# Kernel optimization log

Measured on AMD Instinct MI355X. Metric: run time of the kernel, lower is better.

Reference implementation:

```python
import jax, jax.numpy as jnp
import numpy as np
import math

D = 1024
L = 4096
B = 4

def setup_inputs() -> dict:
    key = jax.random.key(0)
    ks = jax.random.split(key, 6)
    x = jax.random.normal(ks[0], (B, L, D), dtype=jnp.float32)
    base_phases = jax.random.normal(ks[1], (L, D), dtype=jnp.float32) * math.pi
    s = 1.0 / math.sqrt(D)
    W_v = jax.random.normal(ks[2], (D, D), dtype=jnp.float32) * s
    b_v = jnp.zeros((D,), dtype=jnp.float32)
    ln_g = jnp.ones((D,), dtype=jnp.float32)
    ln_b = jnp.zeros((D,), dtype=jnp.float32)
    W_o = jax.random.normal(ks[3], (D, D), dtype=jnp.float32) * s
    b_o = jnp.zeros((D,), dtype=jnp.float32)
    return {"x": x, "base_phases": base_phases, "W_v": W_v, "b_v": b_v,
            "ln_g": ln_g, "ln_b": ln_b, "W_o": W_o, "b_o": b_o}

def _layernorm(x, g, b, eps=1e-5):
    mu = jnp.mean(x, axis=-1, keepdims=True)
    var = jnp.mean(jnp.square(x - mu), axis=-1, keepdims=True)
    return (x - mu) * jax.lax.rsqrt(var + eps) * g + b

def reference(x, base_phases, W_v, b_v, ln_g, ln_b, W_o, b_o):
    Bv, Lv, Dv = x.shape
    phases = base_phases[:Lv][None, :, :]          # [1, L, D]
    cosp, sinp = jnp.cos(phases), jnp.sin(phases)
    value = jnp.einsum('bld,ed->ble', x, W_v) + b_v  # Linear(D,D)
    mem_real = jnp.cumsum(value * cosp, axis=1)
    mem_imag = jnp.cumsum(value * sinp, axis=1)
    retrieved = (mem_real * cosp + mem_imag * sinp) / math.sqrt(Dv)
    out = jnp.einsum('bld,ed->ble', _layernorm(retrieved, ln_g, ln_b), W_o) + b_o
    return x + out
```

## Files before the change

### kernel.cpp

```cpp
#include <hip/hip_runtime.h>
#include <stdint.h>


#define D_DIM 1024
#define L_DIM 4096
#define B_DIM 4
#define M_DIM (B_DIM * L_DIM)
#define CHUNK 64
#define NCH (L_DIM / CHUNK)
#define NT 16

typedef __attribute__((ext_vector_type(8))) short short8;
typedef __attribute__((ext_vector_type(4))) float f32x4;

__device__ __forceinline__ float bf2f(uint32_t h) {
  union { uint32_t u; float f; } x; x.u = h << 16; return x.f;
}
__device__ __forceinline__ uint16_t f2bf(float f) {
  union { float f; uint32_t u; } x; x.f = f;
  uint32_t u = x.u;
  u += 0x7fffu + ((u >> 16) & 1u);
  return (uint16_t)(u >> 16);
}

__global__ void k_f2bf(const float* __restrict__ in, uint16_t* __restrict__ out, int n) {
  int i = (blockIdx.x * 256 + threadIdx.x) * 8;
  if (i >= n) return;
  float4 a = *(const float4*)(in + i);
  float4 b = *(const float4*)(in + i + 4);
  ushort4 o0 = { f2bf(a.x), f2bf(a.y), f2bf(a.z), f2bf(a.w) };
  ushort4 o1 = { f2bf(b.x), f2bf(b.y), f2bf(b.z), f2bf(b.w) };
  *(ushort4*)(out + i) = o0;
  *(ushort4*)(out + i + 4) = o1;
}

__global__ void k_prep_wo(const float* __restrict__ Wo, const float* __restrict__ g,
                          const float* __restrict__ bln, const float* __restrict__ bo,
                          uint16_t* __restrict__ wob, float* __restrict__ u,
                          float* __restrict__ vb) {
  int e = blockIdx.x;
  int tid = threadIdx.x;
  int d = tid * 4;
  float4 w  = *(const float4*)(Wo + (size_t)e * D_DIM + d);
  float4 gg = *(const float4*)(g + d);
  float4 bb = *(const float4*)(bln + d);
  float gw0 = gg.x * w.x, gw1 = gg.y * w.y, gw2 = gg.z * w.z, gw3 = gg.w * w.w;
  ushort4 o = { f2bf(gw0), f2bf(gw1), f2bf(gw2), f2bf(gw3) };
  *(ushort4*)(wob + (size_t)e * D_DIM + d) = o;
  float su = gw0 + gw1 + gw2 + gw3;
  float sv = bb.x * w.x + bb.y * w.y + bb.z * w.z + bb.w * w.w;
#pragma unroll
  for (int off = 32; off > 0; off >>= 1) {
    su += __shfl_down(su, off);
    sv += __shfl_down(sv, off);
  }
  __shared__ float s1[4], s2[4];
  int wid = tid >> 6, lane = tid & 63;
  if (lane == 0) { s1[wid] = su; s2[wid] = sv; }
  __syncthreads();
  if (tid == 0) {
    u[e]  = s1[0] + s1[1] + s1[2] + s1[3];
    vb[e] = s2[0] + s2[1] + s2[2] + s2[3] + bo[e];
  }
}

template <int MODE>
__global__ __launch_bounds__(512, 2) void k_gemm(
    const uint16_t* __restrict__ A, const uint16_t* __restrict__ W,
    void* __restrict__ outp,
    const float* __restrict__ p0, const float* __restrict__ p1,
    const float* __restrict__ mu, const float* __restrict__ inv,
    const uint16_t* __restrict__ xres) {
  __shared__ char lds[8 * 16384];
  const int tid = threadIdx.x;
  const int lane = tid & 63;
  const int wid = tid >> 6;
  const int wm = wid >> 2;
  const int wn = wid & 3;

  const int idx = blockIdx.x;
  const int bm = (idx & 7) * 8 + ((idx >> 3) >> 2);
  const int bn = (idx >> 3) & 3;

  const int srow = tid >> 3;
  const int scb  = (tid & 7) * 16;
  const int scbs = scb ^ ((srow & 7) << 4);

#define GLL(SRC, DST)                                                            \
  __builtin_amdgcn_global_load_lds((const __attribute__((address_space(1))) void*)(SRC), \
                                   (__attribute__((address_space(3))) void*)(DST), 16, 0, 0)

#define STAGE_A(KS, HA)                                                          \
  do {                                                                           \
    char* _d = lds + ((((KS)&1) * 4 + (HA)) << 14) + tid * 16;                   \
    const char* _s = (const char*)A +                                            \
        (size_t)(bm * 256 + (HA) * 128 + srow) * 2048 + (KS) * 128 + scbs;       \
    GLL(_s, _d);                                                                 \
    GLL(_s + (size_t)64 * 2048, _d + 8192);                                      \
  } while (0)

#define STAGE_B(KS, HB)                                                          \
  do {                                                                           \
    char* _d = lds + ((((KS)&1) * 4 + 2 + (HB)) << 14) + tid * 16;               \
    const char* _s = (const char*)W +                                            \
        (size_t)(bn * 256 + (HB) * 128 + srow) * 2048 + (KS) * 128 + scbs;       \
    GLL(_s, _d);                                                                 \
    GLL(_s + (size_t)64 * 2048, _d + 8192);                                      \
  } while (0)

  const int axor = (lane & 7) << 4;
  const int afr  = lane & 15;
  const int acol = (lane >> 4) * 16;

#define LD_A(PAR, I, KK)                                                         \
  (*(const short8*)(lds + (((PAR) * 4 + wm) << 14) + ((I) * 16 + afr) * 128 +    \
                    (((KK) * 64 + acol) ^ axor)))
#define LD_B(PAR, J, KK)                                                         \
  (*(const short8*)(lds + (((PAR) * 4 + 2 + (wn >> 1)) << 14) +                  \
                    ((wn & 1) * 64 + (J) * 16 + afr) * 128 +                     \
                    (((KK) * 64 + acol) ^ axor)))

  f32x4 acc[8][4];
#pragma unroll
  for (int i = 0; i < 8; ++i)
#pragma unroll
    for (int j = 0; j < 4; ++j)
      acc[i][j] = (f32x4){0.f, 0.f, 0.f, 0.f};

  STAGE_A(0, 0); STAGE_A(0, 1);
  STAGE_B(0, 0); STAGE_B(0, 1);
  STAGE_A(1, 0); STAGE_A(1, 1);
  asm volatile("s_waitcnt vmcnt(4)" ::: "memory");
  __builtin_amdgcn_s_barrier();

  for (int ks = 0; ks < NT; ++ks) {
    const int par = ks & 1;
    short8 a0, a1, a2, a3, b0, b1, b2, b3;

    b0 = LD_B(par, 0, 0); b1 = LD_B(par, 1, 0); b2 = LD_B(par, 2, 0); b3 = LD_B(par, 3, 0);
    a0 = LD_A(par, 0, 0); a1 = LD_A(par, 1, 0); a2 = LD_A(par, 2, 0); a3 = LD_A(par, 3, 0);
    if (ks + 1 < NT) STAGE_B(ks + 1, 0);
    __builtin_amdgcn_s_barrier();
    asm volatile("s_waitcnt lgkmcnt(0)" ::: "memory");
    __builtin_amdgcn_sched_barrier(0);
    __builtin_amdgcn_s_setprio(1);
#pragma unroll
    for (int j = 0; j < 4; ++j) {
      const short8 bj = (j == 0) ? b0 : (j == 1) ? b1 : (j == 2) ? b2 : b3;
      acc[0][j] = __builtin_amdgcn_mfma_f32_16x16x32_bf16(a0, bj, acc[0][j], 0, 0, 0);
      acc[1][j] = __builtin_amdgcn_mfma_f32_16x16x32_bf16(a1, bj, acc[1][j], 0, 0, 0);
      acc[2][j] = __builtin_amdgcn_mfma_f32_16x16x32_bf16(a2, bj, acc[2][j], 0, 0, 0);
      acc[3][j] = __builtin_amdgcn_mfma_f32_16x16x32_bf16(a3, bj, acc[3][j], 0, 0, 0);
    }
    __builtin_amdgcn_s_setprio(0);
    __builtin_amdgcn_s_barrier();

    a0 = LD_A(par, 4, 0); a1 = LD_A(par, 5, 0); a2 = LD_A(par, 6, 0); a3 = LD_A(par, 7, 0);
    if (ks + 1 < NT) STAGE_B(ks + 1, 1);
    __builtin_amdgcn_s_barrier();
    asm volatile("s_waitcnt lgkmcnt(0)" ::: "memory");
    __builtin_amdgcn_sched_barrier(0);
    __builtin_amdgcn_s_setprio(1);
#pragma unroll
    for (int j = 0; j < 4; ++j) {
      const short8 bj = (j == 0) ? b0 : (j == 1) ? b1 : (j == 2) ? b2 : b3;
      acc[4][j] = __builtin_amdgcn_mfma_f32_16x16x32_bf16(a0, bj, acc[4][j], 0, 0, 0);
      acc[5][j] = __builtin_amdgcn_mfma_f32_16x16x32_bf16(a1, bj, acc[5][j], 0, 0, 0);
      acc[6][j] = __builtin_amdgcn_mfma_f32_16x16x32_bf16(a2, bj, acc[6][j], 0, 0, 0);
      acc[7][j] = __builtin_amdgcn_mfma_f32_16x16x32_bf16(a3, bj, acc[7][j], 0, 0, 0);
    }
    __builtin_amdgcn_s_setprio(0);
    __builtin_amdgcn_s_barrier();

    b0 = LD_B(par, 0, 1); b1 = LD_B(par, 1, 1); b2 = LD_B(par, 2, 1); b3 = LD_B(par, 3, 1);
    a0 = LD_A(par, 0, 1); a1 = LD_A(par, 1, 1); a2 = LD_A(par, 2, 1); a3 = LD_A(par, 3, 1);
    __builtin_amdgcn_s_barrier();
    asm volatile("s_waitcnt lgkmcnt(0)" ::: "memory");
    __builtin_amdgcn_sched_barrier(0);
    __builtin_amdgcn_s_setprio(1);
#pragma unroll
    for (int j = 0; j < 4; ++j) {
      const short8 bj = (j == 0) ? b0 : (j == 1) ? b1 : (j == 2) ? b2 : b3;
      acc[0][j] = __builtin_amdgcn_mfma_f32_16x16x32_bf16(a0, bj, acc[0][j], 0, 0, 0);
      acc[1][j] = __builtin_amdgcn_mfma_f32_16x16x32_bf16(a1, bj, acc[1][j], 0, 0, 0);
      acc[2][j] = __builtin_amdgcn_mfma_f32_16x16x32_bf16(a2, bj, acc[2][j], 0, 0, 0);
      acc[3][j] = __builtin_amdgcn_mfma_f32_16x16x32_bf16(a3, bj, acc[3][j], 0, 0, 0);
    }
    __builtin_amdgcn_s_setprio(0);
    __builtin_amdgcn_s_barrier();

    a0 = LD_A(par, 4, 1); a1 = LD_A(par, 5, 1); a2 = LD_A(par, 6, 1); a3 = LD_A(par, 7, 1);
    asm volatile("s_waitcnt lgkmcnt(0)" ::: "memory");
    __builtin_amdgcn_sched_barrier(0);
    __builtin_amdgcn_s_barrier();
    __builtin_amdgcn_sched_barrier(0);
    if (ks + 2 < NT) { STAGE_A(ks + 2, 0); STAGE_A(ks + 2, 1); }
    __builtin_amdgcn_s_setprio(1);
#pragma unroll
    for (int j = 0; j < 4; ++j) {
      const short8 bj = (j == 0) ? b0 : (j == 1) ? b1 : (j == 2) ? b2 : b3;
      acc[4][j] = __builtin_amdgcn_mfma_f32_16x16x32_bf16(a0, bj, acc[4][j], 0, 0, 0);
      acc[5][j] = __builtin_amdgcn_mfma_f32_16x16x32_bf16(a1, bj, acc[5][j], 0, 0, 0);
      acc[6][j] = __builtin_amdgcn_mfma_f32_16x16x32_bf16(a2, bj, acc[6][j], 0, 0, 0);
      acc[7][j] = __builtin_amdgcn_mfma_f32_16x16x32_bf16(a3, bj, acc[7][j], 0, 0, 0);
    }
    __builtin_amdgcn_s_setprio(0);
    if (ks == NT - 2) { asm volatile("s_waitcnt vmcnt(0)" ::: "memory"); }
    else              { asm volatile("s_waitcnt vmcnt(4)" ::: "memory"); }
    __builtin_amdgcn_s_barrier();
  }

  if (MODE == 0) {
    uint16_t* outv = (uint16_t*)outp;
    __syncthreads();
#pragma unroll
    for (int i = 0; i < 8; ++i)
#pragma unroll
      for (int r = 0; r < 4; ++r) {
        int row = wm * 128 + i * 16 + (lane >> 4) * 4 + r;
#pragma unroll
        for (int j = 0; j < 4; ++j) {
          int ncol = wn * 64 + j * 16 + (lane & 15);
          float v = acc[i][j][r] + p0[bn * 256 + ncol];
          *(uint16_t*)(lds + row * 512 + ((ncol * 2) ^ ((row & 7) << 4))) = f2bf(v);
        }
      }
    __syncthreads();
    {
      int row = tid >> 1, half = tid & 1;
      uint16_t* gdst = outv + (size_t)(bm * 256 + row) * D_DIM + bn * 256 + half * 128;
#pragma unroll
      for (int s = 0; s < 16; ++s) {
        short8 v = *(const short8*)(lds + row * 512 +
                                    ((half * 256 + s * 16) ^ ((row & 7) << 4)));
        *(short8*)(gdst + s * 8) = v;
      }
    }
  } else {
    float* outf = (float*)outp;
#pragma unroll
    for (int i = 0; i < 8; ++i)
#pragma unroll
      for (int r = 0; r < 4; ++r) {
        int m = bm * 256 + wm * 128 + i * 16 + (lane >> 4) * 4 + r;
        float im = inv[m], mm = mu[m];
#pragma unroll
        for (int j = 0; j < 4; ++j) {
          int n = bn * 256 + wn * 64 + j * 16 + (lane & 15);
          outf[(size_t)m * D_DIM + n] =
              im * acc[i][j][r] - im * mm * p0[n] + p1[n] +
              bf2f(xres[(size_t)m * D_DIM + n]);
        }
      }
  }
#undef GLL
#undef STAGE_A
#undef STAGE_B
#undef LD_A
#undef LD_B
}

__global__ void k_passA(const uint16_t* __restrict__ value, const float* __restrict__ phases,
                        float* __restrict__ pr, float* __restrict__ pi) {
  int d0 = blockIdx.x * 512 + threadIdx.x * 2;
  int c = blockIdx.y, b = blockIdx.z;
  const uint16_t* vp = value + ((size_t)(b * L_DIM + c * CHUNK)) * D_DIM + d0;
  const float* pp = phases + (size_t)(c * CHUNK) * D_DIM + d0;
  float sr0 = 0, si0 = 0, sr1 = 0, si1 = 0;
#pragma unroll 4
  for (int l = 0; l < CHUNK; ++l) {
    uint32_t vv = *(const uint32_t*)vp; vp += D_DIM;
    float2 ph = *(const float2*)pp; pp += D_DIM;
    float v0 = bf2f(vv & 0xffffu), v1 = bf2f(vv >> 16);
    float s0, c0, s1, c1;
    __sincosf(ph.x, &s0, &c0);
    __sincosf(ph.y, &s1, &c1);
    sr0 += v0 * c0; si0 += v0 * s0;
    sr1 += v1 * c1; si1 += v1 * s1;
  }
  size_t o = ((size_t)b * NCH + c) * D_DIM + d0;
  *(float2*)(pr + o) = make_float2(sr0, sr1);
  *(float2*)(pi + o) = make_float2(si0, si1);
}

__global__ void k_passB(float* __restrict__ pr, float* __restrict__ pi) {
  int d = blockIdx.x * 256 + threadIdx.x;
  int b = blockIdx.y;
  size_t base = (size_t)b * NCH * D_DIM + d;
  float r[NCH], im[NCH];
#pragma unroll
  for (int c = 0; c < NCH; ++c) r[c] = pr[base + (size_t)c * D_DIM];
#pragma unroll
  for (int c = 0; c < NCH; ++c) im[c] = pi[base + (size_t)c * D_DIM];
  float rr = 0, ri = 0;
#pragma unroll
  for (int c = 0; c < NCH; ++c) {
    float t = r[c]; r[c] = rr; rr += t;
    t = im[c]; im[c] = ri; ri += t;
  }
#pragma unroll
  for (int c = 0; c < NCH; ++c) pr[base + (size_t)c * D_DIM] = r[c];
#pragma unroll
  for (int c = 0; c < NCH; ++c) pi[base + (size_t)c * D_DIM] = im[c];
}

__global__ void k_passC(const uint16_t* __restrict__ value, const float* __restrict__ phases,
                        const float* __restrict__ pr, const float* __restrict__ pi,
                        uint16_t* __restrict__ ret) {
  int d0 = blockIdx.x * 512 + threadIdx.x * 2;
  int c = blockIdx.y, b = blockIdx.z;
  size_t o = ((size_t)b * NCH + c) * D_DIM + d0;
  float2 r0 = *(const float2*)(pr + o);
  float2 i0 = *(const float2*)(pi + o);
  float mr0 = r0.x, mr1 = r0.y, mi0 = i0.x, mi1 = i0.y;
  size_t rowoff = ((size_t)(b * L_DIM + c * CHUNK)) * D_DIM + d0;
  const uint16_t* vp = value + rowoff;
  uint16_t* rp = ret + rowoff;
  const float* pp = phases + (size_t)(c * CHUNK) * D_DIM + d0;
  const float isd = 0.03125f;
#pragma unroll 4
  for (int l = 0; l < CHUNK; ++l) {
    uint32_t vv = *(const uint32_t*)vp; vp += D_DIM;
    float2 ph = *(const float2*)pp; pp += D_DIM;
    float v0 = bf2f(vv & 0xffffu), v1 = bf2f(vv >> 16);
    float s0, c0, s1, c1;
    __sincosf(ph.x, &s0, &c0);
    __sincosf(ph.y, &s1, &c1);
    mr0 += v0 * c0; mi0 += v0 * s0;
    mr1 += v1 * c1; mi1 += v1 * s1;
    float o0 = (mr0 * c0 + mi0 * s0) * isd;
    float o1 = (mr1 * c1 + mi1 * s1) * isd;
    *(uint32_t*)rp = (uint32_t)f2bf(o0) | ((uint32_t)f2bf(o1) << 16);
    rp += D_DIM;
  }
}

__global__ void k_stats(const uint16_t* __restrict__ ret, float* __restrict__ mu,
                        float* __restrict__ inv) {
  int m = blockIdx.x, tid = threadIdx.x;
  ushort4 v = *(const ushort4*)(ret + (size_t)m * D_DIM + tid * 4);
  float f0 = bf2f(v.x), f1 = bf2f(v.y), f2_ = bf2f(v.z), f3 = bf2f(v.w);
  float s = f0 + f1 + f2_ + f3;
  float ss = f0 * f0 + f1 * f1 + f2_ * f2_ + f3 * f3;
#pragma unroll
  for (int off = 32; off > 0; off >>= 1) {
    s += __shfl_down(s, off);
    ss += __shfl_down(ss, off);
  }
  __shared__ float a1[4], a2[4];
  int wid = tid >> 6, lane = tid & 63;
  if (lane == 0) { a1[wid] = s; a2[wid] = ss; }
  __syncthreads();
  if (tid == 0) {
    float S = a1[0] + a1[1] + a1[2] + a1[3];
    float SS = a2[0] + a2[1] + a2[2] + a2[3];
    float mm = S * (1.0f / 1024.0f);
    float var = SS * (1.0f / 1024.0f) - mm * mm;
    mu[m] = mm;
    inv[m] = rsqrtf(var + 1e-5f);
  }
}

extern "C" void kernel_launch(void* const* d_in, const int* in_sizes, int n_in,
                              void* d_out, int out_size, void* d_ws, size_t ws_size,
                              hipStream_t stream) {
  const float* x      = (const float*)d_in[0];
  const float* phases = (const float*)d_in[1];
  const float* Wv     = (const float*)d_in[2];
  const float* bv     = (const float*)d_in[3];
  const float* lng    = (const float*)d_in[4];
  const float* lnb    = (const float*)d_in[5];
  const float* Wo     = (const float*)d_in[6];
  const float* bo     = (const float*)d_in[7];
  float* out = (float*)d_out;

  char* ws = (char*)d_ws;
  uint16_t* xb    = (uint16_t*)(ws);
  uint16_t* value = (uint16_t*)(ws + (32ull << 20));
  uint16_t* wv    = (uint16_t*)(ws + (64ull << 20));
  uint16_t* wob   = (uint16_t*)(ws + (66ull << 20));
  float* pr       = (float*)(ws + (68ull << 20));
  float* pi       = (float*)(ws + (69ull << 20));
  float* u        = (float*)(ws + (70ull << 20));
  float* vb       = (float*)(ws + (70ull << 20) + 4096);
  float* mu       = (float*)(ws + (71ull << 20));
  float* inv      = (float*)(ws + (72ull << 20));
  uint16_t* retr  = value;

  k_f2bf<<<(M_DIM * D_DIM) / 8 / 256, 256, 0, stream>>>(x, xb, M_DIM * D_DIM);
  k_f2bf<<<(D_DIM * D_DIM) / 8 / 256, 256, 0, stream>>>(Wv, wv, D_DIM * D_DIM);
  k_prep_wo<<<D_DIM, 256, 0, stream>>>(Wo, lng, lnb, bo, wob, u, vb);
  k_gemm<0><<<(M_DIM / 256) * (D_DIM / 256), 512, 0, stream>>>(
      xb, wv, value, bv, nullptr, nullptr, nullptr, nullptr);
  k_passA<<<dim3(2, NCH, B_DIM), 256, 0, stream>>>(value, phases, pr, pi);
  k_passB<<<dim3(D_DIM / 256, B_DIM), 256, 0, stream>>>(pr, pi);
  k_passC<<<dim3(2, NCH, B_DIM), 256, 0, stream>>>(value, phases, pr, pi, retr);
  k_stats<<<M_DIM, 256, 0, stream>>>(retr, mu, inv);
  k_gemm<1><<<(M_DIM / 256) * (D_DIM / 256), 512, 0, stream>>>(
      retr, wob, out, u, vb, mu, inv, xb);
}
```

Baseline: 152.6 us.

## Merge prep kernels and restructure GEMM LDS loads for deeper prefetch

The three preprocessing launches (x and Wv bf16 conversion, Wo folding) become a single kernel that dispatches work by block index, removing two launch gaps. In the GEMM main loop, both k-halves of the A and B fragments are now read from LDS up front and waited on with partial lgkmcnt counts, so the MFMAs on the first half can start while the second half's reads are still in flight. Both global B stages are issued together and fewer workgroup barriers are used per iteration. This raises register pressure from the extra fragment registers and depends on the LDS read counters being ordered as the partial waits assume.

```diff
diff --git a/kernel.cpp b/kernel.cpp
--- a/kernel.cpp
+++ b/kernel.cpp
@@ -23,23 +23,28 @@
   return (uint16_t)(u >> 16);
 }
 
-__global__ void k_f2bf(const float* __restrict__ in, uint16_t* __restrict__ out, int n) {
-  int i = (blockIdx.x * 256 + threadIdx.x) * 8;
-  if (i >= n) return;
-  float4 a = *(const float4*)(in + i);
-  float4 b = *(const float4*)(in + i + 4);
-  ushort4 o0 = { f2bf(a.x), f2bf(a.y), f2bf(a.z), f2bf(a.w) };
-  ushort4 o1 = { f2bf(b.x), f2bf(b.y), f2bf(b.z), f2bf(b.w) };
-  *(ushort4*)(out + i) = o0;
-  *(ushort4*)(out + i + 4) = o1;
-}
-
-__global__ void k_prep_wo(const float* __restrict__ Wo, const float* __restrict__ g,
-                          const float* __restrict__ bln, const float* __restrict__ bo,
-                          uint16_t* __restrict__ wob, float* __restrict__ u,
-                          float* __restrict__ vb) {
-  int e = blockIdx.x;
+__global__ void k_prep(const float* __restrict__ x, const float* __restrict__ Wv,
+                       const float* __restrict__ Wo, const float* __restrict__ g,
+                       const float* __restrict__ bln, const float* __restrict__ bo,
+                       uint16_t* __restrict__ xb, uint16_t* __restrict__ wv,
+                       uint16_t* __restrict__ wob, float* __restrict__ u,
+                       float* __restrict__ vb) {
+  int blk = blockIdx.x;
   int tid = threadIdx.x;
+  if (blk < 8192 + 512) {
+    const float* in = (blk < 8192) ? x : Wv;
+    uint16_t* outp = (blk < 8192) ? xb : wv;
+    int base = (blk < 8192) ? blk : (blk - 8192);
+    int i = (base * 256 + tid) * 8;
+    float4 a = *(const float4*)(in + i);
+    float4 b = *(const float4*)(in + i + 4);
+    ushort4 o0 = { f2bf(a.x), f2bf(a.y), f2bf(a.z), f2bf(a.w) };
+    ushort4 o1 = { f2bf(b.x), f2bf(b.y), f2bf(b.z), f2bf(b.w) };
+    *(ushort4*)(outp + i) = o0;
+    *(ushort4*)(outp + i + 4) = o1;
+    return;
+  }
+  int e = blk - 8704;
   int d = tid * 4;
   float4 w  = *(const float4*)(Wo + (size_t)e * D_DIM + d);
   float4 gg = *(const float4*)(g + d);
@@ -120,6 +125,8 @@
                     ((wn & 1) * 64 + (J) * 16 + afr) * 128 +                     \
                     (((KK) * 64 + acol) ^ axor)))
 
+#define MFMA(AV, BV, CV) __builtin_amdgcn_mfma_f32_16x16x32_bf16(AV, BV, CV, 0, 0, 0)
+
   f32x4 acc[8][4];
 #pragma unroll
   for (int i = 0; i < 8; ++i)
@@ -135,61 +142,57 @@
 
   for (int ks = 0; ks < NT; ++ks) {
     const int par = ks & 1;
-    short8 a0, a1, a2, a3, b0, b1, b2, b3;
-
-    b0 = LD_B(par, 0, 0); b1 = LD_B(par, 1, 0); b2 = LD_B(par, 2, 0); b3 = LD_B(par, 3, 0);
-    a0 = LD_A(par, 0, 0); a1 = LD_A(par, 1, 0); a2 = LD_A(par, 2, 0); a3 = LD_A(par, 3, 0);
-    if (ks + 1 < NT) STAGE_B(ks + 1, 0);
+    short8 A00, A01, A02, A03, A10, A11, A12, A13;
+    short8 B00, B01, B02, B03, B10, B11, B12, B13;
+
+    B00 = LD_B(par, 0, 0); B01 = LD_B(par, 1, 0); B02 = LD_B(par, 2, 0); B03 = LD_B(par, 3, 0);
+    A00 = LD_A(par, 0, 0); A01 = LD_A(par, 1, 0); A02 = LD_A(par, 2, 0); A03 = LD_A(par, 3, 0);
+    __builtin_amdgcn_sched_barrier(0);
+    B10 = LD_B(par, 0, 1); B11 = LD_B(par, 1, 1); B12 = LD_B(par, 2, 1); B13 = LD_B(par, 3, 1);
+    A10 = LD_A(par, 0, 1); A11 = LD_A(par, 1, 1); A12 = LD_A(par, 2, 1); A13 = LD_A(par, 3, 1);
+    __builtin_amdgcn_sched_barrier(0);
+    if (ks + 1 < NT) { STAGE_B(ks + 1, 0); STAGE_B(ks + 1, 1); }
     __builtin_amdgcn_s_barrier();
+    asm volatile("s_waitcnt lgkmcnt(8)" ::: "memory");
+    __builtin_amdgcn_sched_barrier(0);
+    __builtin_amdgcn_s_setprio(1);
+#pragma unroll
+    for (int j = 0; j < 4; ++j) {
+      const short8 bj = (j == 0) ? B00 : (j == 1) ? B01 : (j == 2) ? B02 : B03;
+      acc[0][j] = MFMA(A00, bj, acc[0][j]);
+      acc[1][j] = MFMA(A01, bj, acc[1][j]);
+      acc[2][j] = MFMA(A02, bj, acc[2][j]);
+      acc[3][j] = MFMA(A03, bj, acc[3][j]);
+    }
     asm volatile("s_waitcnt lgkmcnt(0)" ::: "memory");
     __builtin_amdgcn_sched_barrier(0);
-    __builtin_amdgcn_s_setprio(1);
 #pragma unroll
     for (int j = 0; j < 4; ++j) {
-      const short8 bj = (j == 0) ? b0 : (j == 1) ? b1 : (j == 2) ? b2 : b3;
-      acc[0][j] = __builtin_amdgcn_mfma_f32_16x16x32_bf16(a0, bj, acc[0][j], 0, 0, 0);
-      acc[1][j] = __builtin_amdgcn_mfma_f32_16x16x32_bf16(a1, bj, acc[1][j], 0, 0, 0);
-      acc[2][j] = __builtin_amdgcn_mfma_f32_16x16x32_bf16(a2, bj, acc[2][j], 0, 0, 0);
-      acc[3][j] = __builtin_amdgcn_mfma_f32_16x16x32_bf16(a3, bj, acc[3][j], 0, 0, 0);
+      const short8 bj = (j == 0) ? B10 : (j == 1) ? B11 : (j == 2) ? B12 : B13;
+      acc[0][j] = MFMA(A10, bj, acc[0][j]);
+      acc[1][j] = MFMA(A11, bj, acc[1][j]);
+      acc[2][j] = MFMA(A12, bj, acc[2][j]);
+      acc[3][j] = MFMA(A13, bj, acc[3][j]);
     }
     __builtin_amdgcn_s_setprio(0);
     __builtin_amdgcn_s_barrier();
 
-    a0 = LD_A(par, 4, 0); a1 = LD_A(par, 5, 0); a2 = LD_A(par, 6, 0); a3 = LD_A(par, 7, 0);
-    if (ks + 1 < NT) STAGE_B(ks + 1, 1);
-    __builtin_amdgcn_s_barrier();
-    asm volatile("s_waitcnt lgkmcnt(0)" ::: "memory");
+    A00 = LD_A(par, 4, 0); A01 = LD_A(par, 5, 0); A02 = LD_A(par, 6, 0); A03 = LD_A(par, 7, 0);
+    __builtin_amdgcn_sched_barrier(0);
+    A10 = LD_A(par, 4, 1); A11 = LD_A(par, 5, 1); A12 = LD_A(par, 6, 1); A13 = LD_A(par, 7, 1);
+    __builtin_amdgcn_sched_barrier(0);
+    asm volatile("s_waitcnt lgkmcnt(4)" ::: "memory");
     __builtin_amdgcn_sched_barrier(0);
     __builtin_amdgcn_s_setprio(1);
 #pragma unroll
     for (int j = 0; j < 4; ++j) {
-      const short8 bj = (j == 0) ? b0 : (j == 1) ? b1 : (j == 2) ? b2 : b3;
-      acc[4][j] = __builtin_amdgcn_mfma_f32_16x16x32_bf16(a0, bj, acc[4][j], 0, 0, 0);
-      acc[5][j] = __builtin_amdgcn_mfma_f32_16x16x32_bf16(a1, bj, acc[5][j], 0, 0, 0);
-      acc[6][j] = __builtin_amdgcn_mfma_f32_16x16x32_bf16(a2, bj, acc[6][j], 0, 0, 0);
-      acc[7][j] = __builtin_amdgcn_mfma_f32_16x16x32_bf16(a3, bj, acc[7][j], 0, 0, 0);
+      const short8 bj = (j == 0) ? B00 : (j == 1) ? B01 : (j == 2) ? B02 : B03;
+      acc[4][j] = MFMA(A00, bj, acc[4][j]);
+      acc[5][j] = MFMA(A01, bj, acc[5][j]);
+      acc[6][j] = MFMA(A02, bj, acc[6][j]);
+      acc[7][j] = MFMA(A03, bj, acc[7][j]);
     }
     __builtin_amdgcn_s_setprio(0);
-    __builtin_amdgcn_s_barrier();
-
-    b0 = LD_B(par, 0, 1); b1 = LD_B(par, 1, 1); b2 = LD_B(par, 2, 1); b3 = LD_B(par, 3, 1);
-    a0 = LD_A(par, 0, 1); a1 = LD_A(par, 1, 1); a2 = LD_A(par, 2, 1); a3 = LD_A(par, 3, 1);
-    __builtin_amdgcn_s_barrier();
-    asm volatile("s_waitcnt lgkmcnt(0)" ::: "memory");
-    __builtin_amdgcn_sched_barrier(0);
-    __builtin_amdgcn_s_setprio(1);
-#pragma unroll
-    for (int j = 0; j < 4; ++j) {
-      const short8 bj = (j == 0) ? b0 : (j == 1) ? b1 : (j == 2) ? b2 : b3;
-      acc[0][j] = __builtin_amdgcn_mfma_f32_16x16x32_bf16(a0, bj, acc[0][j], 0, 0, 0);
-      acc[1][j] = __builtin_amdgcn_mfma_f32_16x16x32_bf16(a1, bj, acc[1][j], 0, 0, 0);
-      acc[2][j] = __builtin_amdgcn_mfma_f32_16x16x32_bf16(a2, bj, acc[2][j], 0, 0, 0);
-      acc[3][j] = __builtin_amdgcn_mfma_f32_16x16x32_bf16(a3, bj, acc[3][j], 0, 0, 0);
-    }
-    __builtin_amdgcn_s_setprio(0);
-    __builtin_amdgcn_s_barrier();
-
-    a0 = LD_A(par, 4, 1); a1 = LD_A(par, 5, 1); a2 = LD_A(par, 6, 1); a3 = LD_A(par, 7, 1);
     asm volatile("s_waitcnt lgkmcnt(0)" ::: "memory");
     __builtin_amdgcn_sched_barrier(0);
     __builtin_amdgcn_s_barrier();
@@ -198,11 +201,11 @@
     __builtin_amdgcn_s_setprio(1);
 #pragma unroll
     for (int j = 0; j < 4; ++j) {
-      const short8 bj = (j == 0) ? b0 : (j == 1) ? b1 : (j == 2) ? b2 : b3;
-      acc[4][j] = __builtin_amdgcn_mfma_f32_16x16x32_bf16(a0, bj, acc[4][j], 0, 0, 0);
-      acc[5][j] = __builtin_amdgcn_mfma_f32_16x16x32_bf16(a1, bj, acc[5][j], 0, 0, 0);
-      acc[6][j] = __builtin_amdgcn_mfma_f32_16x16x32_bf16(a2, bj, acc[6][j], 0, 0, 0);
-      acc[7][j] = __builtin_amdgcn_mfma_f32_16x16x32_bf16(a3, bj, acc[7][j], 0, 0, 0);
+      const short8 bj = (j == 0) ? B10 : (j == 1) ? B11 : (j == 2) ? B12 : B13;
+      acc[4][j] = MFMA(A10, bj, acc[4][j]);
+      acc[5][j] = MFMA(A11, bj, acc[5][j]);
+      acc[6][j] = MFMA(A12, bj, acc[6][j]);
+      acc[7][j] = MFMA(A13, bj, acc[7][j]);
     }
     __builtin_amdgcn_s_setprio(0);
     if (ks == NT - 2) { asm volatile("s_waitcnt vmcnt(0)" ::: "memory"); }
@@ -258,6 +261,7 @@
 #undef STAGE_B
 #undef LD_A
 #undef LD_B
+#undef MFMA
 }
 
 __global__ void k_passA(const uint16_t* __restrict__ value, const float* __restrict__ phases,
@@ -387,9 +391,8 @@
   float* inv      = (float*)(ws + (72ull << 20));
   uint16_t* retr  = value;
 
-  k_f2bf<<<(M_DIM * D_DIM) / 8 / 256, 256, 0, stream>>>(x, xb, M_DIM * D_DIM);
-  k_f2bf<<<(D_DIM * D_DIM) / 8 / 256, 256, 0, stream>>>(Wv, wv, D_DIM * D_DIM);
-  k_prep_wo<<<D_DIM, 256, 0, stream>>>(Wo, lng, lnb, bo, wob, u, vb);
+  k_prep<<<8192 + 512 + 1024, 256, 0, stream>>>(x, Wv, Wo, lng, lnb, bo,
+                                                xb, wv, wob, u, vb);
   k_gemm<0><<<(M_DIM / 256) * (D_DIM / 256), 512, 0, stream>>>(
       xb, wv, value, bv, nullptr, nullptr, nullptr, nullptr);
   k_passA<<<dim3(2, NCH, B_DIM), 256, 0, stream>>>(value, phases, pr, pi);
```

Measured after the change: 146.8 us (median of 2 runs). 3.8% less time.
